# Kernel tuning notes

Hardware: AMD Instinct MI355X
Metric: run time of the kernel (lower is better)

## Reference

```python
import jax, jax.numpy as jnp
import numpy as np
import math

B, S, D, H = 8, 1024, 512, 8
DH = D // H
SCALE_BASE = 512


def _xpos(x, downscale):
    # x: [B, H, S, DH]; xpos rotary with exponential scale (jamie-stirling RetNet impl)
    s = x.shape[-2]
    d = x.shape[-1]
    half = d // 2
    sv = (jnp.arange(0, d, 2, dtype=jnp.float32) + 0.4 * d) / (1.4 * d)      # [half]
    power = jnp.arange(s, dtype=jnp.float32) / SCALE_BASE
    scale = sv[None, :] ** power[:, None]                                     # [s, half]
    inv_freq = 1.0 / (10000.0 ** (jnp.arange(half, dtype=jnp.float32) / half))
    ang = jnp.arange(s, dtype=jnp.float32)[:, None] * inv_freq[None, :]       # [s, half]
    if downscale:
        scale = 1.0 / scale
    sin = jnp.repeat(jnp.sin(ang) * scale, 2, axis=-1)                        # [s, d]
    cos = jnp.repeat(jnp.cos(ang) * scale, 2, axis=-1)
    rot = jnp.stack((-x[..., 1::2], x[..., ::2]), axis=-1).reshape(x.shape)   # rotate_every_two
    return x * cos + rot * sin


def setup_inputs() -> dict:
    key = jax.random.key(0)
    ks = jax.random.split(key, 7)
    X = jax.random.normal(ks[0], (B, S, D), dtype=jnp.float32)
    # per-head projections stacked: torch init randn/hidden_size
    W_Q = jax.random.normal(ks[1], (H, D, DH), dtype=jnp.float32) / D
    W_K = jax.random.normal(ks[2], (H, D, DH), dtype=jnp.float32) / D
    W_V = jax.random.normal(ks[3], (H, D, DH), dtype=jnp.float32) / D
    W_G = jax.random.normal(ks[4], (D, D), dtype=jnp.float32) / D
    W_O = jax.random.normal(ks[5], (D, D), dtype=jnp.float32) / D
    gn_weight = jnp.ones((D,), dtype=jnp.float32)
    gn_bias = jnp.zeros((D,), dtype=jnp.float32)
    return {"X": X, "W_Q": W_Q, "W_K": W_K, "W_V": W_V, "W_G": W_G,
            "W_O": W_O, "gn_weight": gn_weight, "gn_bias": gn_bias}


def reference(X, W_Q, W_K, W_V, W_G, W_O, gn_weight, gn_bias):
    b, s, _ = X.shape
    # per-head decay gammas and symmetric (non-causal) decay matrix D
    gammas = 1.0 - jnp.exp(jnp.linspace(math.log(1.0 / 32), math.log(1.0 / 512), H)).astype(jnp.float32)
    n = jnp.arange(s)
    Dmat = gammas[:, None, None] ** jnp.abs(n[:, None] - n[None, :]).astype(jnp.float32)  # [H,s,s]
    Q = _xpos(jnp.einsum('bsd,hde->bhse', X, W_Q), False)
    K = _xpos(jnp.einsum('bsd,hde->bhse', X, W_K), True)
    V = jnp.einsum('bsd,hde->bhse', X, W_V)
    scores = jnp.einsum('bhse,bhte->bhst', Q, K)
    p = jax.nn.softmax(scores, axis=-1) * Dmat[None]          # decay-weighted softmax
    Y = jnp.einsum('bhst,bhte->bhse', p, V)                    # [b,H,s,DH]
    Y = jnp.moveaxis(Y, 1, 2).reshape(b, s, H * DH)            # concat heads -> [b,s,D]
    # GroupNorm(H groups) over flattened rows [b*s, D]
    Yg = Y.reshape(-1, H, DH)
    mu = Yg.mean(axis=-1, keepdims=True)
    var = Yg.var(axis=-1, keepdims=True)
    Yn = ((Yg - mu) * jax.lax.rsqrt(var + 1e-5)).reshape(-1, H * DH)
    Yn = (Yn * gn_weight + gn_bias).reshape(b, s, H * DH)
    G = X @ W_G
    swish = G * jax.nn.sigmoid(G)
    return (swish * Yn) @ W_O
```

## Files before the change

kernel.cpp:

```cpp
#include <hip/hip_runtime.h>
#include <math.h>

#define B_ 8
#define S_ 1024
#define D_ 512
#define H_ 8
#define DH_ 64
#define M_ (B_*S_)

typedef __attribute__((ext_vector_type(8))) short short8;
typedef __attribute__((ext_vector_type(4))) short s16x4;
typedef __attribute__((ext_vector_type(4))) float f32x4;
typedef __attribute__((ext_vector_type(4))) unsigned int u32x4;

__device__ inline void tsplit(float x, short& hs, short& ls) {
  unsigned u = __float_as_uint(x);
  hs = (short)(u >> 16);
  float r = x - __uint_as_float(u & 0xFFFF0000u);
  ls = (short)(__float_as_uint(r) >> 16);
}
__device__ inline void splitpack(f32x4 a, f32x4 b, short8& hh, short8& ll) {
  union { u32x4 u; short8 s; } H, L;
#pragma unroll
  for (int j = 0; j < 2; ++j) {
    unsigned u0 = __float_as_uint(a[2 * j]);
    unsigned u1 = __float_as_uint(a[2 * j + 1]);
    H.u[j] = (u0 >> 16) | (u1 & 0xFFFF0000u);
    float r0 = a[2 * j]     - __uint_as_float(u0 & 0xFFFF0000u);
    float r1 = a[2 * j + 1] - __uint_as_float(u1 & 0xFFFF0000u);
    L.u[j] = (__float_as_uint(r0) >> 16) | (__float_as_uint(r1) & 0xFFFF0000u);
    unsigned v0 = __float_as_uint(b[2 * j]);
    unsigned v1 = __float_as_uint(b[2 * j + 1]);
    H.u[2 + j] = (v0 >> 16) | (v1 & 0xFFFF0000u);
    float s0 = b[2 * j]     - __uint_as_float(v0 & 0xFFFF0000u);
    float s1 = b[2 * j + 1] - __uint_as_float(v1 & 0xFFFF0000u);
    L.u[2 + j] = (__float_as_uint(s0) >> 16) | (__float_as_uint(s1) & 0xFFFF0000u);
  }
  hh = H.s; ll = L.s;
}
__device__ inline f32x4 mfma16(short8 a, short8 b, f32x4 c) {
  return __builtin_amdgcn_mfma_f32_16x16x32_bf16(a, b, c, 0, 0, 0);
}
__device__ inline void gload_lds16(const void* g, void* l) {
  __builtin_amdgcn_global_load_lds(
      (const __attribute__((address_space(1))) void*)g,
      (__attribute__((address_space(3))) void*)l, 16, 0, 0);
}


__global__ void xpos_table_kernel(float* __restrict__ tab) {
  int idx = blockIdx.x * 256 + threadIdx.x;
  int s = idx >> 5, i = idx & 31;
  float sv = (2.0f * (float)i + 0.4f * 64.0f) / (1.4f * 64.0f);
  float p = (float)s / 512.0f;
  float scale = powf(sv, p);
  float inv_freq = powf(10000.0f, -((float)i / 32.0f));
  float ang = (float)s * inv_freq;
  float sn = sinf(ang), cs = cosf(ang);
  tab[idx]          = cs * scale;
  tab[32768 + idx]  = sn * scale;
  tab[65536 + idx]  = cs / scale;
  tab[98304 + idx]  = sn / scale;
}

__global__ __launch_bounds__(256) void wprep_kernel(
    const float* __restrict__ Wq, const float* __restrict__ Wk,
    const float* __restrict__ Wv, const float* __restrict__ Wg,
    short* __restrict__ BTh, short* __restrict__ BTl, int gonly) {
  __shared__ float t[64][65];
  const int n0 = blockIdx.x * 64, k0 = blockIdx.y * 64;
  const int tid = threadIdx.x;
  const float* src;
  int ld;
  if (gonly) {
    src = Wg + (size_t)k0 * 512 + n0; ld = 512;
  } else {
    int w = n0 >> 9, nn = n0 & 511;
    if (w == 3) { src = Wg + (size_t)k0 * 512 + nn; ld = 512; }
    else {
      const float* W = (w == 0) ? Wq : ((w == 1) ? Wk : Wv);
      int h = nn >> 6;
      src = W + (size_t)h * D_ * DH_ + (size_t)k0 * 64; ld = 64;
    }
  }
#pragma unroll
  for (int i = 0; i < 4; ++i) {
    int idx = tid + i * 256;
    int kk = idx >> 4, nl4 = (idx & 15) * 4;
    float4 v = *(const float4*)(src + (size_t)kk * ld + nl4);
    t[kk][nl4] = v.x; t[kk][nl4 + 1] = v.y; t[kk][nl4 + 2] = v.z; t[kk][nl4 + 3] = v.w;
  }
  __syncthreads();
#pragma unroll
  for (int i = 0; i < 2; ++i) {
    int idx = tid + i * 256;
    int nl = idx >> 3, ck = idx & 7;
    short8 hh, ll;
#pragma unroll
    for (int j = 0; j < 8; ++j) {
      short h_, l_;
      tsplit(t[ck * 8 + j][nl], h_, l_);
      hh[j] = h_; ll[j] = l_;
    }
    const int n = n0 + nl, k = k0 + ck * 8;
    const size_t off = ((size_t)((n >> 7) * 16 + (k >> 5))) * 4096
                     + (size_t)((n >> 4) & 7) * 512
                     + (size_t)(((k >> 3) & 3) * 16 + (n & 15)) * 8;
    *(short8*)(BTh + off) = hh;
    *(short8*)(BTl + off) = ll;
  }
}

template<int AMODE, int NSUB>
__global__ __launch_bounds__(256, 2) void gemm_mfma_kernel(
    const float* __restrict__ Af,
    const short* __restrict__ Ah, const short* __restrict__ Al,
    const short* __restrict__ BTh, const short* __restrict__ BTl,
    const float* __restrict__ tab,
    short* __restrict__ QhO, short* __restrict__ QlO,
    short* __restrict__ KhO, short* __restrict__ KlO,
    short* __restrict__ VhT, short* __restrict__ VlT,
    float* __restrict__ G) {
  constexpr int NT = NSUB * 32;
  constexpr int BSZ = NT * 32;
  constexpr int AFSZ = (AMODE == 0) ? 2 * 4096 : 4;
  constexpr int ASSZ = (AMODE == 1) ? 2 * 4096 : 4;
  __shared__ __align__(16) float AsF[AFSZ];
  __shared__ __align__(16) short AsH[ASSZ], AsL[ASSZ];
  __shared__ __align__(16) short BsH[2 * BSZ], BsL[2 * BSZ];
  const int m0 = blockIdx.x * 128, by = blockIdx.y;
  const int tid = threadIdx.x, w = tid >> 6, lane = tid & 63;
  const int lx = lane & 15, quad = lane >> 4;
  const int wr = w >> 1, wc = w & 1;
  f32x4 acc[4][NSUB] = {};

  auto stage = [&](int bsel, int kt) {
    if constexpr (AMODE == 0) {
      const int r8 = lane >> 3, cg = (lane & 7) ^ r8;
      const float* ab = Af + (size_t)(m0 + r8) * 512 + kt * 32 + cg * 4;
      float* ad = &AsF[bsel * 4096];
#pragma unroll
      for (int c = 0; c < 4; ++c) {
        const int ch = w * 4 + c;
        gload_lds16(ab + (size_t)ch * (8 * 512), ad + ch * 256);
      }
    } else {
      const size_t ta = ((size_t)blockIdx.x * 16 + kt) * 4096 + lane * 8;
      gload_lds16(Ah + ta + (size_t)w * 512,       &AsH[bsel * 4096 + w * 512]);
      gload_lds16(Ah + ta + (size_t)(w + 4) * 512, &AsH[bsel * 4096 + (w + 4) * 512]);
      gload_lds16(Al + ta + (size_t)w * 512,       &AsL[bsel * 4096 + w * 512]);
      gload_lds16(Al + ta + (size_t)(w + 4) * 512, &AsL[bsel * 4096 + (w + 4) * 512]);
    }
    if constexpr (NSUB == 4) {
      const size_t tb = ((size_t)by * 16 + kt) * 4096 + lane * 8;
      gload_lds16(BTh + tb + (size_t)w * 512,       &BsH[bsel * BSZ + w * 512]);
      gload_lds16(BTh + tb + (size_t)(w + 4) * 512, &BsH[bsel * BSZ + (w + 4) * 512]);
      gload_lds16(BTl + tb + (size_t)w * 512,       &BsL[bsel * BSZ + w * 512]);
      gload_lds16(BTl + tb + (size_t)(w + 4) * 512, &BsL[bsel * BSZ + (w + 4) * 512]);
    } else {
      const size_t tb = ((size_t)(by >> 1) * 16 + kt) * 4096
                      + (size_t)(by & 1) * 2048 + lane * 8;
      const short* src = (w < 2) ? BTh : BTl;
      short* dst = (w < 2) ? &BsH[bsel * BSZ] : &BsL[bsel * BSZ];
      const int wq = (w & 1) * 2;
      gload_lds16(src + tb + (size_t)wq * 512,       dst + wq * 512);
      gload_lds16(src + tb + (size_t)(wq + 1) * 512, dst + (wq + 1) * 512);
    }
  };

  stage(0, 0);
  int cur = 0;
  for (int t = 0; t < 16; ++t) {
    asm volatile("s_waitcnt lgkmcnt(0)" ::: "memory");
    __builtin_amdgcn_s_barrier();
    asm volatile("" ::: "memory");
    if (t < 15) {
      stage(cur ^ 1, t + 1);
      if constexpr (AMODE == 0)
        asm volatile("s_waitcnt vmcnt(8)" ::: "memory");
      else
        asm volatile("s_waitcnt vmcnt(6)" ::: "memory");
    } else {
      asm volatile("s_waitcnt vmcnt(0)" ::: "memory");
    }
    __builtin_amdgcn_s_barrier();
    asm volatile("" ::: "memory");

    short8 fah[4], fal[4], fbh[NSUB], fbl[NSUB];
    if constexpr (AMODE == 0) {
      const float* ab = &AsF[cur * 4096];
#pragma unroll
      for (int i = 0; i < 4; ++i) {
        const int row = wr * 64 + i * 16 + lx;
        f32x4 x0 = *(const f32x4*)(ab + row * 32 + (((quad * 2)     ^ (lx & 7)) * 4));
        f32x4 x1 = *(const f32x4*)(ab + row * 32 + (((quad * 2 + 1) ^ (lx & 7)) * 4));
        splitpack(x0, x1, fah[i], fal[i]);
      }
    } else {
#pragma unroll
      for (int i = 0; i < 4; ++i) {
        fah[i] = *(const short8*)&AsH[cur * 4096 + (wr * 4 + i) * 512 + lane * 8];
        fal[i] = *(const short8*)&AsL[cur * 4096 + (wr * 4 + i) * 512 + lane * 8];
      }
    }
#pragma unroll
    for (int i = 0; i < NSUB; ++i) {
      const int g = (NSUB == 4 ? wc * 4 : wc * 2) + i;
      fbh[i] = *(const short8*)&BsH[cur * BSZ + g * 512 + lane * 8];
      fbl[i] = *(const short8*)&BsL[cur * BSZ + g * 512 + lane * 8];
    }
#pragma unroll
    for (int ms = 0; ms < 4; ++ms)
#pragma unroll
      for (int ns = 0; ns < NSUB; ++ns) {
        f32x4 a = acc[ms][ns];
        a = mfma16(fah[ms], fbh[ns], a);
        a = mfma16(fal[ms], fbh[ns], a);
        a = mfma16(fah[ms], fbl[ns], a);
        acc[ms][ns] = a;
      }
    cur ^= 1;
  }
  if constexpr (AMODE == 0) {
    const int w4 = by >> 2;
    const int ncb = (by & 3) * 128 + wc * 64;
    if (w4 < 2) {
      short* Ph = (w4 == 0) ? QhO : KhO;
      short* Pl = (w4 == 0) ? QlO : KlO;
      const float* ct = tab + (w4 ? 65536 : 0);
      const float* st = tab + (w4 ? 98304 : 32768);
#pragma unroll
      for (int ms = 0; ms < 4; ++ms) {
        const int m = m0 + wr * 64 + ms * 16 + quad * 4;
        const int b = m >> 10, sbase = m & 1023;
#pragma unroll
        for (int ns = 0; ns < 4; ++ns) {
          const int n = ncb + ns * 16 + lx;
          const int h = n >> 6, e = n & 63;
          const int i0 = e >> 1;
          const float sgn = (e & 1) ? 1.0f : -1.0f;
          short* ph = Ph + (((size_t)(b * 8 + h)) * 1024 + sbase) * 64 + e;
          short* pl = Pl + (((size_t)(b * 8 + h)) * 1024 + sbase) * 64 + e;
#pragma unroll
          for (int rg = 0; rg < 4; ++rg) {
            const int s = sbase + rg;
            float v = acc[ms][ns][rg];
            float vp = __shfl_xor(v, 1);
            float o = v * ct[s * 32 + i0] + sgn * vp * st[s * 32 + i0];
            short h_, l_;
            tsplit(o, h_, l_);
            ph[rg * 64] = h_;
            pl[rg * 64] = l_;
          }
        }
      }
    } else if (w4 == 2) {
#pragma unroll
      for (int ms = 0; ms < 4; ++ms) {
        const int m = m0 + wr * 64 + ms * 16 + quad * 4;
        const int b = m >> 10, s = m & 1023;
#pragma unroll
        for (int ns = 0; ns < 4; ++ns) {
          const int n = ncb + ns * 16 + lx;
          const int h = n >> 6, e = n & 63;
          s16x4 hh, ll;
#pragma unroll
          for (int rg = 0; rg < 4; ++rg) {
            short h_, l_;
            tsplit(acc[ms][ns][rg], h_, l_);
            hh[rg] = h_; ll[rg] = l_;
          }
          size_t off = (((size_t)(b * 8 + h)) * 64 + e) * 1024 + s;
          *(s16x4*)(VhT + off) = hh;
          *(s16x4*)(VlT + off) = ll;
        }
      }
    } else {
#pragma unroll
      for (int ms = 0; ms < 4; ++ms) {
        const int m = m0 + wr * 64 + ms * 16 + quad * 4;
#pragma unroll
        for (int ns = 0; ns < 4; ++ns) {
          const int n = ncb + ns * 16 + lx;
#pragma unroll
          for (int rg = 0; rg < 4; ++rg) G[(size_t)(m + rg) * 512 + n] = acc[ms][ns][rg];
        }
      }
    }
  } else {
#pragma unroll
    for (int ms = 0; ms < 4; ++ms) {
      const int m = m0 + wr * 64 + ms * 16 + quad * 4;
#pragma unroll
      for (int ns = 0; ns < NSUB; ++ns) {
        const int n = by * NT + wc * (NSUB * 16) + ns * 16 + lx;
#pragma unroll
        for (int rg = 0; rg < 4; ++rg) G[(size_t)(m + rg) * 512 + n] = acc[ms][ns][rg];
      }
    }
  }
}

__global__ __launch_bounds__(256, 2) void attn_mfma_kernel(
    const short* __restrict__ Qh, const short* __restrict__ Ql,
    const short* __restrict__ Kh, const short* __restrict__ Kl,
    const short* __restrict__ VhT, const short* __restrict__ VlT,
    const float* __restrict__ Gp,
    const float* __restrict__ gnw, const float* __restrict__ gnb,
    short* __restrict__ Zh, short* __restrict__ Zl) {
  __shared__ __align__(16) short KhS[64][72];
  __shared__ __align__(16) short KlS[64][72];
  __shared__ __align__(16) short VhS[64][72];
  __shared__ __align__(16) short VlS[64][72];
  __shared__ __align__(16) short PhS[4][32][72];
  const int bh = blockIdx.x, s0 = blockIdx.y * 128;
  const int b = bh >> 3, h = bh & 7;
  const int tid = threadIdx.x;
  const int w = tid >> 6, lane = tid & 63;
  const int lx = lane & 15, quad = lane >> 4;
  const int s0w = s0 + w * 32;
  const float l0c = -3.4657359027997265f;
  const float l1c = -6.2383246250395075f;
  const float gamma = 1.0f - expf(l0c + (float)h * (l1c - l0c) / 7.0f);
  const float lg2g = log2f(gamma);
  const short* Qbh = Qh + (size_t)bh * S_ * DH_;
  const short* Qbl = Ql + (size_t)bh * S_ * DH_;
  const short* Kbh = Kh + (size_t)bh * S_ * DH_;
  const short* Kbl = Kl + (size_t)bh * S_ * DH_;
  const short* VbH = VhT + (size_t)bh * DH_ * S_;
  const short* VbL = VlT + (size_t)bh * DH_ * S_;

  float cl[4], cr[4], w4g[4], b4g[4];
#pragma unroll
  for (int ns = 0; ns < 4; ++ns) {
    cl[ns] = exp2f(lg2g * (float)(ns * 16 + lx));
    cr[ns] = exp2f(lg2g * (float)(63 - ns * 16 - lx));
    w4g[ns] = gnw[h * DH_ + ns * 16 + lx];
    b4g[ns] = gnb[h * DH_ + ns * 16 + lx];
  }

  short8 qfh[2][2], qfl[2][2];
#pragma unroll
  for (int ms = 0; ms < 2; ++ms)
#pragma unroll
    for (int kc = 0; kc < 2; ++kc) {
      size_t off = (size_t)(s0w + ms * 16 + lx) * DH_ + kc * 32 + quad * 8;
      qfh[ms][kc] = *(const short8*)(Qbh + off);
      qfl[ms][kc] = *(const short8*)(Qbl + off);
    }

  f32x4 O[2][4] = {};
  float lsum[2][4] = {};

  for (int t0 = 0; t0 < S_; t0 += 64) {
    __syncthreads();
#pragma unroll
    for (int i = 0; i < 2; ++i) {
      int slot = tid + i * 256;
      int r = slot >> 3, c8 = (slot & 7) * 8;
      *(short8*)&KhS[r][c8] = *(const short8*)(Kbh + (size_t)(t0 + r) * DH_ + c8);
      *(short8*)&KlS[r][c8] = *(const short8*)(Kbl + (size_t)(t0 + r) * DH_ + c8);
      *(short8*)&VhS[r][c8] = *(const short8*)(VbH + (size_t)r * S_ + t0 + c8);
      *(short8*)&VlS[r][c8] = *(const short8*)(VbL + (size_t)r * S_ + t0 + c8);
    }
    __syncthreads();
    f32x4 acc[2][4];
#pragma unroll
    for (int ns = 0; ns < 4; ++ns) {
      short8 kh0 = *(const short8*)&KhS[ns * 16 + lx][quad * 8];
      short8 kh1 = *(const short8*)&KhS[ns * 16 + lx][32 + quad * 8];
      short8 kl0 = *(const short8*)&KlS[ns * 16 + lx][quad * 8];
      short8 kl1 = *(const short8*)&KlS[ns * 16 + lx][32 + quad * 8];
#pragma unroll
      for (int ms = 0; ms < 2; ++ms) {
        f32x4 a = {};
        a = mfma16(qfh[ms][0], kh0, a);
        a = mfma16(qfl[ms][0], kh0, a);
        a = mfma16(qfh[ms][0], kl0, a);
        a = mfma16(qfh[ms][1], kh1, a);
        a = mfma16(qfl[ms][1], kh1, a);
        a = mfma16(qfh[ms][1], kl1, a);
        acc[ms][ns] = a;
      }
    }
    const int cse = (t0 + 63 < s0w) ? 0 : ((t0 > s0w + 31) ? 1 : 2);
#pragma unroll
    for (int ms = 0; ms < 2; ++ms)
#pragma unroll
      for (int rg = 0; rg < 4; ++rg) {
        const int rloc = ms * 16 + quad * 4 + rg;
        const int srow = s0w + rloc;
        float pe[4], p[4];
#pragma unroll
        for (int ns = 0; ns < 4; ++ns) pe[ns] = __expf(acc[ms][ns][rg]);
        lsum[ms][rg] += (pe[0] + pe[1]) + (pe[2] + pe[3]);
        if (cse == 0) {
          float rf = exp2f(lg2g * (float)(srow - t0 - 63));
#pragma unroll
          for (int ns = 0; ns < 4; ++ns) p[ns] = pe[ns] * rf * cr[ns];
        } else if (cse == 1) {
          float rf = exp2f(lg2g * (float)(t0 - srow));
#pragma unroll
          for (int ns = 0; ns < 4; ++ns) p[ns] = pe[ns] * rf * cl[ns];
        } else {
#pragma unroll
          for (int ns = 0; ns < 4; ++ns)
            p[ns] = pe[ns] * exp2f(lg2g * fabsf((float)(srow - (t0 + ns * 16 + lx))));
        }
#pragma unroll
        for (int ns = 0; ns < 4; ++ns)
          PhS[w][rloc][ns * 16 + lx] = (short)((__float_as_uint(p[ns]) + 0x8000u) >> 16);
      }
    short8 pf[2][2];
#pragma unroll
    for (int ms = 0; ms < 2; ++ms)
#pragma unroll
      for (int kc = 0; kc < 2; ++kc)
        pf[ms][kc] = *(const short8*)&PhS[w][ms * 16 + lx][kc * 32 + quad * 8];
#pragma unroll
    for (int ns = 0; ns < 4; ++ns) {
      short8 vh0 = *(const short8*)&VhS[ns * 16 + lx][quad * 8];
      short8 vh1 = *(const short8*)&VhS[ns * 16 + lx][32 + quad * 8];
      short8 vl0 = *(const short8*)&VlS[ns * 16 + lx][quad * 8];
      short8 vl1 = *(const short8*)&VlS[ns * 16 + lx][32 + quad * 8];
#pragma unroll
      for (int ms = 0; ms < 2; ++ms) {
        f32x4 o = O[ms][ns];
        o = mfma16(pf[ms][0], vh0, o);
        o = mfma16(pf[ms][0], vl0, o);
        o = mfma16(pf[ms][1], vh1, o);
        o = mfma16(pf[ms][1], vl1, o);
        O[ms][ns] = o;
      }
    }
  }
#pragma unroll
  for (int ms = 0; ms < 2; ++ms)
#pragma unroll
    for (int rg = 0; rg < 4; ++rg) {
      float s = lsum[ms][rg];
      s += __shfl_xor(s, 1);
      s += __shfl_xor(s, 2);
      s += __shfl_xor(s, 4);
      s += __shfl_xor(s, 8);
      const float inv = 1.0f / s;
      const int srow = s0w + ms * 16 + quad * 4 + rg;
      float y[4];
      float rs = 0.0f;
#pragma unroll
      for (int ns = 0; ns < 4; ++ns) { y[ns] = O[ms][ns][rg] * inv; rs += y[ns]; }
      rs += __shfl_xor(rs, 1);
      rs += __shfl_xor(rs, 2);
      rs += __shfl_xor(rs, 4);
      rs += __shfl_xor(rs, 8);
      const float mu = rs * (1.0f / 64.0f);
      float vv = 0.0f;
#pragma unroll
      for (int ns = 0; ns < 4; ++ns) { float d = y[ns] - mu; vv += d * d; }
      vv += __shfl_xor(vv, 1);
      vv += __shfl_xor(vv, 2);
      vv += __shfl_xor(vv, 4);
      vv += __shfl_xor(vv, 8);
      const float rstd = rsqrtf(vv * (1.0f / 64.0f) + 1e-5f);
      const size_t base = (size_t)(b * S_ + srow) * D_ + h * DH_;
      const int m = b * S_ + srow;
      const size_t zb = ((size_t)((m >> 7) * 16 + h * 2)) * 4096
                      + (size_t)((m >> 4) & 7) * 512 + (size_t)(m & 15) * 8;
#pragma unroll
      for (int ns = 0; ns < 4; ++ns) {
        float g = Gp[base + ns * 16 + lx];
        float sw = g / (1.0f + __expf(-g));
        float z = sw * ((y[ns] - mu) * rstd * w4g[ns] + b4g[ns]);
        short zh_, zl_;
        tsplit(z, zh_, zl_);
        const size_t off = zb + (size_t)(ns >> 1) * 4096
                         + (size_t)(((ns * 2 + (lx >> 3)) & 3) * 128) + (lx & 7);
        Zh[off] = zh_;
        Zl[off] = zl_;
      }
    }
}

extern "C" void kernel_launch(void* const* d_in, const int* in_sizes, int n_in,
                              void* d_out, int out_size, void* d_ws, size_t ws_size,
                              hipStream_t stream) {
  const float* X   = (const float*)d_in[0];
  const float* Wq  = (const float*)d_in[1];
  const float* Wk  = (const float*)d_in[2];
  const float* Wv  = (const float*)d_in[3];
  const float* Wg  = (const float*)d_in[4];
  const float* Wo  = (const float*)d_in[5];
  const float* gnw = (const float*)d_in[6];
  const float* gnb = (const float*)d_in[7];
  float* out = (float*)d_out;
  float* ws  = (float*)d_ws;
  const size_t NB = (size_t)M_ * D_;
  float* R0 = ws;
  float* R1 = ws + NB;
  float* R2 = ws + 2 * NB;
  float* R3 = ws + 3 * NB;
  float* tab = ws + 4 * NB;
  short* BTh = (short*)R3;
  short* BTl = BTh + (size_t)2048 * 512;
  short* Qh = (short*)R0;  short* Ql = Qh + NB;
  short* Kh = (short*)R1;  short* Kl = Kh + NB;
  short* VhT = (short*)R2; short* VlT = VhT + NB;
  short* Zh = (short*)R3;  short* Zl = Zh + NB;
  short* BToh = (short*)R1;
  short* BTol = BToh + (size_t)512 * 512;

  wprep_kernel<<<dim3(32, 8), 256, 0, stream>>>(Wq, Wk, Wv, Wg, BTh, BTl, 0);
  xpos_table_kernel<<<128, 256, 0, stream>>>(tab);
  gemm_mfma_kernel<0, 4><<<dim3(64, 16), 256, 0, stream>>>(
      X, nullptr, nullptr, BTh, BTl, tab, Qh, Ql, Kh, Kl, VhT, VlT, out);
  attn_mfma_kernel<<<dim3(64, 8), 256, 0, stream>>>(
      Qh, Ql, Kh, Kl, VhT, VlT, out, gnw, gnb, Zh, Zl);
  wprep_kernel<<<dim3(8, 8), 256, 0, stream>>>(nullptr, nullptr, nullptr, Wo, BToh, BTol, 1);
  gemm_mfma_kernel<1, 2><<<dim3(64, 8), 256, 0, stream>>>(
      nullptr, Zh, Zl, BToh, BTol, nullptr, nullptr, nullptr, nullptr, nullptr,
      nullptr, nullptr, out);
}
```

Baseline: 223.3 us.

## Pre-split X into bf16 hi/lo tiles and double-buffer attention K/V loads

Adds a kernel that splits X into hi/lo bf16 halves once, stored in the GEMM tile layout. The first GEMM then streams pre-split tiles instead of converting fp32 in every one of the 16 column blocks that reread X. The attention kernel now stages K/V asynchronously into double-buffered LDS with a XOR swizzle, and the P scratch uses the same swizzle, so global loads overlap compute and bank conflicts drop. The cost is an extra launch plus extra workspace traffic for Xh/Xl.

```diff
diff --git a/kernel.cpp b/kernel.cpp
--- a/kernel.cpp
+++ b/kernel.cpp
@@ -61,6 +61,26 @@
   tab[32768 + idx]  = sn * scale;
   tab[65536 + idx]  = cs / scale;
   tab[98304 + idx]  = sn / scale;
+}
+
+__global__ __launch_bounds__(256) void xsplit_kernel(
+    const float* __restrict__ X, short* __restrict__ Xh, short* __restrict__ Xl) {
+  const int tid = threadIdx.x;
+  const size_t tile = ((size_t)blockIdx.x * 16 + blockIdx.y) * 4096;
+#pragma unroll
+  for (int i = 0; i < 2; ++i) {
+    int idx = tid + i * 256;
+    int g = idx >> 6, sl = idx & 63;
+    int m = blockIdx.x * 128 + g * 16 + (sl & 15);
+    int k = blockIdx.y * 32 + (sl >> 4) * 8;
+    const float* xp = X + (size_t)m * 512 + k;
+    f32x4 a = *(const f32x4*)xp;
+    f32x4 b = *(const f32x4*)(xp + 4);
+    short8 hh, ll;
+    splitpack(a, b, hh, ll);
+    *(short8*)(Xh + tile + (size_t)idx * 8) = hh;
+    *(short8*)(Xl + tile + (size_t)idx * 8) = ll;
+  }
 }
 
 __global__ __launch_bounds__(256) void wprep_kernel(
@@ -111,9 +131,8 @@
   }
 }
 
-template<int AMODE, int NSUB>
+template<int NSUB, int FUSED>
 __global__ __launch_bounds__(256, 2) void gemm_mfma_kernel(
-    const float* __restrict__ Af,
     const short* __restrict__ Ah, const short* __restrict__ Al,
     const short* __restrict__ BTh, const short* __restrict__ BTl,
     const float* __restrict__ tab,
@@ -123,10 +142,7 @@
     float* __restrict__ G) {
   constexpr int NT = NSUB * 32;
   constexpr int BSZ = NT * 32;
-  constexpr int AFSZ = (AMODE == 0) ? 2 * 4096 : 4;
-  constexpr int ASSZ = (AMODE == 1) ? 2 * 4096 : 4;
-  __shared__ __align__(16) float AsF[AFSZ];
-  __shared__ __align__(16) short AsH[ASSZ], AsL[ASSZ];
+  __shared__ __align__(16) short AsH[2 * 4096], AsL[2 * 4096];
   __shared__ __align__(16) short BsH[2 * BSZ], BsL[2 * BSZ];
   const int m0 = blockIdx.x * 128, by = blockIdx.y;
   const int tid = threadIdx.x, w = tid >> 6, lane = tid & 63;
@@ -135,22 +151,11 @@
   f32x4 acc[4][NSUB] = {};
 
   auto stage = [&](int bsel, int kt) {
-    if constexpr (AMODE == 0) {
-      const int r8 = lane >> 3, cg = (lane & 7) ^ r8;
-      const float* ab = Af + (size_t)(m0 + r8) * 512 + kt * 32 + cg * 4;
-      float* ad = &AsF[bsel * 4096];
-#pragma unroll
-      for (int c = 0; c < 4; ++c) {
-        const int ch = w * 4 + c;
-        gload_lds16(ab + (size_t)ch * (8 * 512), ad + ch * 256);
-      }
-    } else {
-      const size_t ta = ((size_t)blockIdx.x * 16 + kt) * 4096 + lane * 8;
-      gload_lds16(Ah + ta + (size_t)w * 512,       &AsH[bsel * 4096 + w * 512]);
-      gload_lds16(Ah + ta + (size_t)(w + 4) * 512, &AsH[bsel * 4096 + (w + 4) * 512]);
-      gload_lds16(Al + ta + (size_t)w * 512,       &AsL[bsel * 4096 + w * 512]);
-      gload_lds16(Al + ta + (size_t)(w + 4) * 512, &AsL[bsel * 4096 + (w + 4) * 512]);
-    }
+    const size_t ta = ((size_t)blockIdx.x * 16 + kt) * 4096 + lane * 8;
+    gload_lds16(Ah + ta + (size_t)w * 512,       &AsH[bsel * 4096 + w * 512]);
+    gload_lds16(Ah + ta + (size_t)(w + 4) * 512, &AsH[bsel * 4096 + (w + 4) * 512]);
+    gload_lds16(Al + ta + (size_t)w * 512,       &AsL[bsel * 4096 + w * 512]);
+    gload_lds16(Al + ta + (size_t)(w + 4) * 512, &AsL[bsel * 4096 + (w + 4) * 512]);
     if constexpr (NSUB == 4) {
       const size_t tb = ((size_t)by * 16 + kt) * 4096 + lane * 8;
       gload_lds16(BTh + tb + (size_t)w * 512,       &BsH[bsel * BSZ + w * 512]);
@@ -176,8 +181,8 @@
     asm volatile("" ::: "memory");
     if (t < 15) {
       stage(cur ^ 1, t + 1);
-      if constexpr (AMODE == 0)
-        asm volatile("s_waitcnt vmcnt(8)" ::: "memory");
+      if constexpr (NSUB == 4)
+        asm volatile("s_waitcnt vmcnt(12)" ::: "memory");
       else
         asm volatile("s_waitcnt vmcnt(6)" ::: "memory");
     } else {
@@ -187,21 +192,10 @@
     asm volatile("" ::: "memory");
 
     short8 fah[4], fal[4], fbh[NSUB], fbl[NSUB];
-    if constexpr (AMODE == 0) {
-      const float* ab = &AsF[cur * 4096];
-#pragma unroll
-      for (int i = 0; i < 4; ++i) {
-        const int row = wr * 64 + i * 16 + lx;
-        f32x4 x0 = *(const f32x4*)(ab + row * 32 + (((quad * 2)     ^ (lx & 7)) * 4));
-        f32x4 x1 = *(const f32x4*)(ab + row * 32 + (((quad * 2 + 1) ^ (lx & 7)) * 4));
-        splitpack(x0, x1, fah[i], fal[i]);
-      }
-    } else {
-#pragma unroll
-      for (int i = 0; i < 4; ++i) {
-        fah[i] = *(const short8*)&AsH[cur * 4096 + (wr * 4 + i) * 512 + lane * 8];
-        fal[i] = *(const short8*)&AsL[cur * 4096 + (wr * 4 + i) * 512 + lane * 8];
-      }
+#pragma unroll
+    for (int i = 0; i < 4; ++i) {
+      fah[i] = *(const short8*)&AsH[cur * 4096 + (wr * 4 + i) * 512 + lane * 8];
+      fal[i] = *(const short8*)&AsL[cur * 4096 + (wr * 4 + i) * 512 + lane * 8];
     }
 #pragma unroll
     for (int i = 0; i < NSUB; ++i) {
@@ -221,7 +215,7 @@
       }
     cur ^= 1;
   }
-  if constexpr (AMODE == 0) {
+  if constexpr (FUSED) {
     const int w4 = by >> 2;
     const int ncb = (by & 3) * 128 + wc * 64;
     if (w4 < 2) {
@@ -308,11 +302,11 @@
     const float* __restrict__ Gp,
     const float* __restrict__ gnw, const float* __restrict__ gnb,
     short* __restrict__ Zh, short* __restrict__ Zl) {
-  __shared__ __align__(16) short KhS[64][72];
-  __shared__ __align__(16) short KlS[64][72];
-  __shared__ __align__(16) short VhS[64][72];
-  __shared__ __align__(16) short VlS[64][72];
-  __shared__ __align__(16) short PhS[4][32][72];
+  __shared__ __align__(16) short KhS[2][4096];
+  __shared__ __align__(16) short KlS[2][4096];
+  __shared__ __align__(16) short VhS[2][4096];
+  __shared__ __align__(16) short VlS[2][4096];
+  __shared__ __align__(16) short PhS[4][2048];
   const int bh = blockIdx.x, s0 = blockIdx.y * 128;
   const int b = bh >> 3, h = bh & 7;
   const int tid = threadIdx.x;
@@ -349,28 +343,53 @@
       qfl[ms][kc] = *(const short8*)(Qbl + off);
     }
 
+  auto stageKV = [&](int bsel, int t0n) {
+    const int rsub = lane >> 3;
+    const int gsw = (lane & 7) ^ (rsub & 7);
+    if (w < 2) {
+      const short* src = ((w == 0) ? Kbh : Kbl) + (size_t)(t0n + rsub) * 64 + gsw * 8;
+      short* dst = (w == 0) ? &KhS[bsel][0] : &KlS[bsel][0];
+#pragma unroll
+      for (int i = 0; i < 8; ++i)
+        gload_lds16(src + (size_t)i * 8 * 64, dst + i * 512);
+    } else {
+      const short* src = ((w == 2) ? VbH : VbL) + (size_t)rsub * 1024 + t0n + gsw * 8;
+      short* dst = (w == 2) ? &VhS[bsel][0] : &VlS[bsel][0];
+#pragma unroll
+      for (int i = 0; i < 8; ++i)
+        gload_lds16(src + (size_t)i * 8 * 1024, dst + i * 512);
+    }
+  };
+
   f32x4 O[2][4] = {};
   float lsum[2][4] = {};
 
-  for (int t0 = 0; t0 < S_; t0 += 64) {
-    __syncthreads();
-#pragma unroll
-    for (int i = 0; i < 2; ++i) {
-      int slot = tid + i * 256;
-      int r = slot >> 3, c8 = (slot & 7) * 8;
-      *(short8*)&KhS[r][c8] = *(const short8*)(Kbh + (size_t)(t0 + r) * DH_ + c8);
-      *(short8*)&KlS[r][c8] = *(const short8*)(Kbl + (size_t)(t0 + r) * DH_ + c8);
-      *(short8*)&VhS[r][c8] = *(const short8*)(VbH + (size_t)r * S_ + t0 + c8);
-      *(short8*)&VlS[r][c8] = *(const short8*)(VbL + (size_t)r * S_ + t0 + c8);
-    }
-    __syncthreads();
+  stageKV(0, 0);
+  int cur = 0;
+  for (int t = 0; t < 16; ++t) {
+    const int t0 = t * 64;
+    asm volatile("s_waitcnt lgkmcnt(0)" ::: "memory");
+    __builtin_amdgcn_s_barrier();
+    asm volatile("" ::: "memory");
+    if (t < 15) {
+      stageKV(cur ^ 1, t0 + 64);
+      asm volatile("s_waitcnt vmcnt(8)" ::: "memory");
+    } else {
+      asm volatile("s_waitcnt vmcnt(0)" ::: "memory");
+    }
+    __builtin_amdgcn_s_barrier();
+    asm volatile("" ::: "memory");
+
     f32x4 acc[2][4];
 #pragma unroll
     for (int ns = 0; ns < 4; ++ns) {
-      short8 kh0 = *(const short8*)&KhS[ns * 16 + lx][quad * 8];
-      short8 kh1 = *(const short8*)&KhS[ns * 16 + lx][32 + quad * 8];
-      short8 kl0 = *(const short8*)&KlS[ns * 16 + lx][quad * 8];
-      short8 kl1 = *(const short8*)&KlS[ns * 16 + lx][32 + quad * 8];
+      const int rowk = ns * 16 + lx, rk = (rowk & 7) << 3;
+      const short* Kc0 = &KhS[cur][rowk * 64];
+      const short* Kc1 = &KlS[cur][rowk * 64];
+      short8 kh0 = *(const short8*)(Kc0 + (((quad) << 3) ^ rk));
+      short8 kh1 = *(const short8*)(Kc0 + (((4 | quad) << 3) ^ rk));
+      short8 kl0 = *(const short8*)(Kc1 + (((quad) << 3) ^ rk));
+      short8 kl1 = *(const short8*)(Kc1 + (((4 | quad) << 3) ^ rk));
 #pragma unroll
       for (int ms = 0; ms < 2; ++ms) {
         f32x4 a = {};
@@ -407,22 +426,30 @@
           for (int ns = 0; ns < 4; ++ns)
             p[ns] = pe[ns] * exp2f(lg2g * fabsf((float)(srow - (t0 + ns * 16 + lx))));
         }
+        const int r7s = rloc & 7;
+        short* Pw = &PhS[w][rloc * 64 + (lx & 7)];
 #pragma unroll
         for (int ns = 0; ns < 4; ++ns)
-          PhS[w][rloc][ns * 16 + lx] = (short)((__float_as_uint(p[ns]) + 0x8000u) >> 16);
+          Pw[(((ns * 2 + (lx >> 3)) ^ r7s) << 3)] =
+              (short)((__float_as_uint(p[ns]) + 0x8000u) >> 16);
       }
     short8 pf[2][2];
 #pragma unroll
-    for (int ms = 0; ms < 2; ++ms)
+    for (int ms = 0; ms < 2; ++ms) {
+      const int rowp = ms * 16 + lx, rp = (rowp & 7) << 3;
 #pragma unroll
       for (int kc = 0; kc < 2; ++kc)
-        pf[ms][kc] = *(const short8*)&PhS[w][ms * 16 + lx][kc * 32 + quad * 8];
+        pf[ms][kc] = *(const short8*)&PhS[w][rowp * 64 + ((((kc * 4 + quad)) << 3) ^ rp)];
+    }
 #pragma unroll
     for (int ns = 0; ns < 4; ++ns) {
-      short8 vh0 = *(const short8*)&VhS[ns * 16 + lx][quad * 8];
-      short8 vh1 = *(const short8*)&VhS[ns * 16 + lx][32 + quad * 8];
-      short8 vl0 = *(const short8*)&VlS[ns * 16 + lx][quad * 8];
-      short8 vl1 = *(const short8*)&VlS[ns * 16 + lx][32 + quad * 8];
+      const int rowv = ns * 16 + lx, rv = (rowv & 7) << 3;
+      const short* Vc0 = &VhS[cur][rowv * 64];
+      const short* Vc1 = &VlS[cur][rowv * 64];
+      short8 vh0 = *(const short8*)(Vc0 + (((quad) << 3) ^ rv));
+      short8 vh1 = *(const short8*)(Vc0 + (((4 | quad) << 3) ^ rv));
+      short8 vl0 = *(const short8*)(Vc1 + (((quad) << 3) ^ rv));
+      short8 vl1 = *(const short8*)(Vc1 + (((4 | quad) << 3) ^ rv));
 #pragma unroll
       for (int ms = 0; ms < 2; ++ms) {
         f32x4 o = O[ms][ns];
@@ -433,6 +460,7 @@
         O[ms][ns] = o;
       }
     }
+    cur ^= 1;
   }
 #pragma unroll
   for (int ms = 0; ms < 2; ++ms)
@@ -502,6 +530,8 @@
   float* tab = ws + 4 * NB;
   short* BTh = (short*)R3;
   short* BTl = BTh + (size_t)2048 * 512;
+  short* Xh  = BTh + (size_t)2 * 2048 * 512;
+  short* Xl  = (short*)(tab + 131072);
   short* Qh = (short*)R0;  short* Ql = Qh + NB;
   short* Kh = (short*)R1;  short* Kl = Kh + NB;
   short* VhT = (short*)R2; short* VlT = VhT + NB;
@@ -511,12 +541,13 @@
 
   wprep_kernel<<<dim3(32, 8), 256, 0, stream>>>(Wq, Wk, Wv, Wg, BTh, BTl, 0);
   xpos_table_kernel<<<128, 256, 0, stream>>>(tab);
-  gemm_mfma_kernel<0, 4><<<dim3(64, 16), 256, 0, stream>>>(
-      X, nullptr, nullptr, BTh, BTl, tab, Qh, Ql, Kh, Kl, VhT, VlT, out);
+  xsplit_kernel<<<dim3(64, 16), 256, 0, stream>>>(X, Xh, Xl);
+  gemm_mfma_kernel<4, 1><<<dim3(64, 16), 256, 0, stream>>>(
+      Xh, Xl, BTh, BTl, tab, Qh, Ql, Kh, Kl, VhT, VlT, out);
   attn_mfma_kernel<<<dim3(64, 8), 256, 0, stream>>>(
       Qh, Ql, Kh, Kl, VhT, VlT, out, gnw, gnb, Zh, Zl);
   wprep_kernel<<<dim3(8, 8), 256, 0, stream>>>(nullptr, nullptr, nullptr, Wo, BToh, BTol, 1);
-  gemm_mfma_kernel<1, 2><<<dim3(64, 8), 256, 0, stream>>>(
-      nullptr, Zh, Zl, BToh, BTol, nullptr, nullptr, nullptr, nullptr, nullptr,
+  gemm_mfma_kernel<2, 0><<<dim3(64, 8), 256, 0, stream>>>(
+      Zh, Zl, BToh, BTol, nullptr, nullptr, nullptr, nullptr, nullptr,
       nullptr, nullptr, out);
 }
```

Result: faster. 214.9 us (-3.7%).
